# Kernel optimization log

Hardware: AMD Instinct MI355X
Metric: run time of the kernel (lower is better)

## Reference

```python
import jax, jax.numpy as jnp
import numpy as np
from jax import lax

B, G, P = 16, 128, 8000   # batch, MAX_GT_BOXES, num proposals
R = 200                   # train_rois_per_image
POS_CAP = int(R * 0.33)   # max positive rois per image = 66
BOX_STD = np.array([0.1, 0.1, 0.2, 0.2], np.float32)


def _make_boxes(k, shape):
    k1, k2, k3, k4 = jax.random.split(k, 4)
    y1 = jax.random.uniform(k1, shape) * 0.6
    x1 = jax.random.uniform(k2, shape) * 0.6
    h = jax.random.uniform(k3, shape) * 0.35 + 0.02
    w = jax.random.uniform(k4, shape) * 0.35 + 0.02
    return jnp.stack([y1, x1, y1 + h, x1 + w], axis=-1)


def setup_inputs() -> dict:
    key = jax.random.key(0)
    kg, kp, kc, kn, km = jax.random.split(key, 5)
    gt4 = _make_boxes(kg, (B, G))
    gt_cnt = jax.random.randint(kc, (B,), 5, G + 1)
    gt_tag = jnp.arange(G)[None, :] < gt_cnt[:, None]
    gt_boxes = jnp.concatenate([gt4, gt_tag[..., None].astype(jnp.float32)], axis=-1)
    cls = jax.random.randint(kn, (B, G), 1, 81)
    gt_class_ids = jnp.stack([cls * gt_tag, gt_tag.astype(jnp.int32)], axis=-1).astype(jnp.int32)
    pr4 = _make_boxes(kp, (B, P))
    pr_cnt = jax.random.randint(km, (B,), P // 2, P + 1)
    pr_tag = jnp.arange(P)[None, :] < pr_cnt[:, None]
    proposals = jnp.concatenate([pr4, pr_tag[..., None].astype(jnp.float32)], axis=-1)
    return {"gt_boxes": gt_boxes, "gt_class_ids": gt_class_ids, "proposals": proposals}


def _iou(gtb, prb):
    # gtb [G,4], prb [P,4] -> [G,P]
    iw = jnp.maximum(0.0, jnp.minimum(gtb[:, None, 3], prb[None, :, 3]) - jnp.maximum(gtb[:, None, 1], prb[None, :, 1]))
    ih = jnp.maximum(0.0, jnp.minimum(gtb[:, None, 2], prb[None, :, 2]) - jnp.maximum(gtb[:, None, 0], prb[None, :, 0]))
    inter = iw * ih
    ag = (gtb[:, 3] - gtb[:, 1]) * (gtb[:, 2] - gtb[:, 0])
    ap = (prb[:, 3] - prb[:, 1]) * (prb[:, 2] - prb[:, 0])
    return inter / (ag[:, None] + ap[None, :] - inter)


def _regress_target(anchors, gt):
    h = anchors[:, 2] - anchors[:, 0]
    w = anchors[:, 3] - anchors[:, 1]
    gh = gt[:, 2] - gt[:, 0]
    gw = gt[:, 3] - gt[:, 1]
    cy = (anchors[:, 2] + anchors[:, 0]) * 0.5
    cx = (anchors[:, 3] + anchors[:, 1]) * 0.5
    gcy = (gt[:, 2] + gt[:, 0]) * 0.5
    gcx = (gt[:, 3] + gt[:, 1]) * 0.5
    dy = (gcy - cy) / h
    dx = (gcx - cx) / w
    dh = jnp.log(jnp.maximum(gh / h, 1e-8))
    dw = jnp.log(jnp.maximum(gw / w, 1e-8))
    return jnp.stack([dy, dx, dh, dw], axis=1) / jnp.asarray(BOX_STD)


def _detect_targets_one(key, gt_boxes, gt_cls, proposals):
    valid_gt = gt_boxes[:, 4] != 0
    valid_pr = proposals[:, 4] != 0
    gtb = gt_boxes[:, :4]
    prb = proposals[:, :4]
    iou = jnp.where(valid_gt[:, None] & valid_pr[None, :], _iou(gtb, prb), -1.0)
    # remove each GT's best proposal from the candidate set (setdiff1d in original)
    gt_argmax = jnp.argmax(iou, axis=1)
    removed = jnp.zeros(P, jnp.int32).at[gt_argmax].max(valid_gt.astype(jnp.int32)) > 0
    iou2 = jnp.where(removed[None, :], -1.0, iou)
    p_max = iou2.max(axis=0)
    p_arg = jnp.argmax(iou2, axis=0)
    keep = (~removed) & valid_pr
    pos_m = keep & (p_max >= 0.5)
    neg_m = keep & (p_max < 0.5)
    # random subsampling (tf.random_shuffle) via uniform scores + top_k
    k1, k2 = jax.random.split(key)
    pos_idx = lax.top_k(jnp.where(pos_m, jax.random.uniform(k1, (P,)), -1.0), POS_CAP)[1]
    neg_idx = lax.top_k(jnp.where(neg_m, jax.random.uniform(k2, (P,)), -1.0), R)[1]
    n_pos = jnp.minimum(pos_m.sum(), POS_CAP)
    n_neg = jnp.minimum(R - n_pos, neg_m.sum())
    slot = jnp.arange(R)
    is_pos = slot < n_pos
    is_real = slot < n_pos + n_neg
    idx = jnp.where(is_pos, pos_idx[jnp.minimum(slot, POS_CAP - 1)], neg_idx[jnp.clip(slot - n_pos, 0, R - 1)])
    rois4 = jnp.where(is_real[:, None], prb[idx], 0.0)
    gsel = p_arg[idx]
    deltas4 = jnp.where(is_pos[:, None], _regress_target(prb[idx], gtb[gsel]), 0.0)
    cls = jnp.where(is_pos, gt_cls[gsel, 0].astype(jnp.float32), 0.0)
    delta_tag = jnp.where(is_pos, 1.0, jnp.where(is_real, -1.0, 0.0))
    deltas = jnp.concatenate([deltas4, delta_tag[:, None]], axis=1)      # [R,5]
    class_ids = jnp.stack([cls, is_real.astype(jnp.float32)], axis=1)    # [R,2]
    rois = jnp.concatenate([rois4, is_real[:, None].astype(jnp.float32)], axis=1)  # [R,5]
    matched = jnp.zeros(G, jnp.int32).at[p_arg].max(pos_m.astype(jnp.int32))
    miss = (valid_gt.sum() - (matched * valid_gt.astype(jnp.int32)).sum()).astype(jnp.float32)
    return deltas, class_ids, rois, miss


def reference(gt_boxes, gt_class_ids, proposals):
    keys = jax.random.split(jax.random.key(42), gt_boxes.shape[0])
    return jax.vmap(_detect_targets_one)(keys, gt_boxes, gt_class_ids, proposals)
```

## Files before the change

### kernel.cpp

```cpp
#include <hip/hip_runtime.h>
#include <stdint.h>

#define Bn 16
#define Gn 128
#define Pn 8000
#define Rn 200
#define POSCAP 66
#define CANDN 1024

typedef unsigned long long u64;

__device__ __forceinline__ void tf2x32(uint32_t k0, uint32_t k1,
                                       uint32_t x0, uint32_t x1,
                                       uint32_t& y0, uint32_t& y1) {
  uint32_t ks0 = k0, ks1 = k1, ks2 = k0 ^ k1 ^ 0x1BD11BDAu;
  x0 += ks0; x1 += ks1;
#define TF_ROUND(r) { x0 += x1; x1 = (x1 << (r)) | (x1 >> (32 - (r))); x1 ^= x0; }
  TF_ROUND(13) TF_ROUND(15) TF_ROUND(26) TF_ROUND(6)
  x0 += ks1; x1 += ks2 + 1u;
  TF_ROUND(17) TF_ROUND(29) TF_ROUND(16) TF_ROUND(24)
  x0 += ks2; x1 += ks0 + 2u;
  TF_ROUND(13) TF_ROUND(15) TF_ROUND(26) TF_ROUND(6)
  x0 += ks0; x1 += ks1 + 3u;
  TF_ROUND(17) TF_ROUND(29) TF_ROUND(16) TF_ROUND(24)
  x0 += ks1; x1 += ks2 + 4u;
  TF_ROUND(13) TF_ROUND(15) TF_ROUND(26) TF_ROUND(6)
  x0 += ks2; x1 += ks0 + 5u;
#undef TF_ROUND
  y0 = x0; y1 = x1;
}

__device__ __forceinline__ float iou_f(float g0, float g1, float g2, float g3, float ag,
                                       float p0, float p1, float p2, float p3) {
  float iw = fmaxf(0.0f, __fsub_rn(fminf(g3, p3), fmaxf(g1, p1)));
  float ih = fmaxf(0.0f, __fsub_rn(fminf(g2, p2), fmaxf(g0, p0)));
  float inter = __fmul_rn(iw, ih);
  float ap = __fmul_rn(__fsub_rn(p3, p1), __fsub_rn(p2, p0));
  return __fdiv_rn(inter, __fsub_rn(__fadd_rn(ag, ap), inter));
}

__global__ __launch_bounds__(256) void k_iou(const float* __restrict__ gt,
                                             const float* __restrict__ pr,
                                             float* __restrict__ pmax,
                                             int* __restrict__ parg,
                                             u64* __restrict__ rowpk) {
  __shared__ float sg[Gn * 5];
  __shared__ u64 srow[Gn];
  int b = blockIdx.y, tid = threadIdx.x;
  for (int i = tid; i < Gn * 5; i += 256) sg[i] = gt[(size_t)b * Gn * 5 + i];
  for (int i = tid; i < Gn; i += 256) srow[i] = 0ull;
  __syncthreads();
  int p = blockIdx.x * 256 + tid;
  float p0 = 0, p1 = 0, p2 = 0, p3 = 0, pv = 0;
  if (p < Pn) {
    const float* pb = pr + ((size_t)b * Pn + p) * 5;
    p0 = pb[0]; p1 = pb[1]; p2 = pb[2]; p3 = pb[3]; pv = pb[4];
  }
  bool valid = (p < Pn) && (pv != 0.0f);
  float best = -2.0f; int bidx = 0;
  int g0 = tid & (Gn - 1);
  for (int it = 0; it < Gn; it++) {
    int g = (g0 + it) & (Gn - 1);
    const float* gb = sg + g * 5;
    if (valid && gb[4] != 0.0f) {
      float ag = __fmul_rn(__fsub_rn(gb[3], gb[1]), __fsub_rn(gb[2], gb[0]));
      float v = iou_f(gb[0], gb[1], gb[2], gb[3], ag, p0, p1, p2, p3);
      if (v > best || (v == best && g < bidx)) { best = v; bidx = g; }
      u64 key = ((u64)__float_as_uint(v) << 32) | (unsigned)(~p);
      atomicMax(&srow[g], key);
    }
  }
  __syncthreads();
  for (int i = tid; i < Gn; i += 256) {
    u64 v = srow[i];
    if (v) atomicMax(&rowpk[(size_t)b * Gn + i], v);
  }
  if (p < Pn) {
    pmax[(size_t)b * Pn + p] = best;
    parg[(size_t)b * Pn + p] = bidx;
  }
}

__global__ __launch_bounds__(1024) void k_select(
    const float* __restrict__ gt, const int* __restrict__ gtc,
    const float* __restrict__ pr, const float* __restrict__ pmax,
    const int* __restrict__ parg, const u64* __restrict__ rowpk,
    float* __restrict__ out) {
  __shared__ uint32_t skey[Pn];
  __shared__ uint32_t hist2[1024];
  __shared__ uint32_t hist1[1024];
  __shared__ u64 cand[CANDN];
  __shared__ uint32_t rembm[Pn / 32 + 1];
  __shared__ int matched[Gn];
  __shared__ int s_npos, s_nneg, s_miss, s_call, s_cpos, s_T2, s_T1;
  __shared__ uint32_t s_keys[4];
  int b = blockIdx.x, tid = threadIdx.x;

  hist2[tid] = 0; hist1[tid] = 0; cand[tid] = 0ull;
  if (tid < Pn / 32 + 1) rembm[tid] = 0;
  if (tid < Gn) matched[tid] = 0;
  if (tid == 0) {
    s_npos = 0; s_nneg = 0; s_miss = 0; s_call = 0; s_cpos = 0;
    s_T2 = 1025; s_T1 = 1025;
    uint32_t kb0, kb1, a0, a1, c0, c1;
    tf2x32(0u, 42u, 0u, (uint32_t)b, kb0, kb1);
    tf2x32(kb0, kb1, 0u, 0u, a0, a1);
    tf2x32(kb0, kb1, 0u, 1u, c0, c1);
    s_keys[0] = a0; s_keys[1] = a1; s_keys[2] = c0; s_keys[3] = c1;
  }
  __syncthreads();

  if (tid < Gn) {
    float gv = gt[((size_t)b * Gn + tid) * 5 + 4];
    u64 pk = rowpk[(size_t)b * Gn + tid];
    if (gv != 0.0f && pk != 0ull) {
      unsigned p = ~(unsigned)(pk & 0xFFFFFFFFull);
      atomicOr(&rembm[p >> 5], 1u << (p & 31));
    }
  }
  __syncthreads();

  uint32_t k10 = s_keys[0], k11 = s_keys[1], k20 = s_keys[2], k21 = s_keys[3];
  const size_t bp = (size_t)b * Pn;
  int lpos = 0, lneg = 0;
  for (int p = tid; p < Pn; p += 1024) {
    float pv = pr[(bp + p) * 5 + 4];
    int rem = (rembm[p >> 5] >> (p & 31)) & 1;
    float pm = pmax[bp + p];
    int cls = 0;
    if (pv != 0.0f && !rem) cls = (pm >= 0.5f) ? 2 : 1;
    uint32_t key = 0;
    if (cls) {
      uint32_t kk0 = (cls == 2) ? k10 : k20, kk1 = (cls == 2) ? k11 : k21;
      uint32_t y0, y1;
      tf2x32(kk0, kk1, 0u, (uint32_t)p, y0, y1);
      uint32_t val = (y0 ^ y1) >> 9;
      key = ((uint32_t)cls << 23) | val;
      if (cls == 2) { lpos++; matched[parg[bp + p]] = 1; atomicAdd(&hist2[val >> 13], 1u); }
      else { lneg++; atomicAdd(&hist1[val >> 13], 1u); }
    }
    skey[p] = key;
  }
  if (lpos) atomicAdd(&s_npos, lpos);
  if (lneg) atomicAdd(&s_nneg, lneg);
  __syncthreads();

  if (tid < 128) {
    bool isP = tid < 64;
    int lane = tid & 63;
    uint32_t* hist = isP ? hist2 : hist1;
    int cnt = isP ? s_npos : s_nneg;
    int cap = isP ? POSCAP : Rn;
    int need = cnt < cap ? cnt : cap;
    int base = 1024 - 16 * (lane + 1);
    int local = 0;
#pragma unroll
    for (int j = 0; j < 16; j++) local += (int)hist[base + j];
    int incl = local;
    for (int d = 1; d < 64; d <<= 1) {
      int o = __shfl_up(incl, d);
      if (lane >= d) incl += o;
    }
    int above = incl - local;
    if (need > 0 && above < need && above + local >= need) {
      int cum = above, T = base;
      for (int j = 15; j >= 0; j--) {
        cum += (int)hist[base + j];
        if (cum >= need) { T = base + j; break; }
      }
      if (isP) s_T2 = T; else s_T1 = T;
    }
  }
  __syncthreads();
  int T2 = s_T2, T1 = s_T1;

  for (int p = tid; p < Pn; p += 1024) {
    uint32_t key = skey[p];
    int cls = (int)(key >> 23);
    if (cls) {
      int bucket = (int)((key & 0x7FFFFFu) >> 13);
      int T = (cls == 2) ? T2 : T1;
      if (bucket >= T) {
        int slot = atomicAdd(&s_call, 1);
        if (slot < CANDN) {
          cand[slot] = ((u64)key << 16) | (uint32_t)((uint16_t)(~p));
          if (cls == 2) atomicAdd(&s_cpos, 1);
        }
      }
    }
  }
  __syncthreads();

  for (unsigned k = 2; k <= CANDN; k <<= 1) {
    for (unsigned j = k >> 1; j > 0; j >>= 1) {
      unsigned i = tid, l = i ^ j;
      if (l > i) {
        u64 av = cand[i], cv = cand[l];
        bool a_first = av > cv;
        bool desc = ((i & k) == 0u);
        if (desc != a_first) { cand[i] = cv; cand[l] = av; }
      }
      __syncthreads();
    }
  }

  int npos = s_npos, nneg = s_nneg, cpos = s_cpos;
  int n_pos = npos < POSCAP ? npos : POSCAP;
  int rems = Rn - n_pos;
  int n_neg = nneg < rems ? nneg : rems;

  float* o_del = out;
  float* o_cls = out + (size_t)Bn * Rn * 5;
  float* o_roi = out + (size_t)Bn * Rn * 7;
  float* o_mis = out + (size_t)Bn * Rn * 12;

  if (tid < Rn) {
    int s = tid;
    bool is_pos = s < n_pos;
    bool is_real = s < n_pos + n_neg;
    float d0 = 0, d1 = 0, d2 = 0, d3 = 0, d4 = 0, c0 = 0, c1 = 0;
    float r0 = 0, r1 = 0, r2 = 0, r3 = 0, r4 = 0;
    if (is_real) {
      int ci = is_pos ? s : (cpos + (s - n_pos));
      u64 ck = cand[ci];
      int p = (int)((~(unsigned)ck) & 0xFFFFu);
      const float* pb = pr + (bp + p) * 5;
      float q0 = pb[0], q1 = pb[1], q2 = pb[2], q3 = pb[3];
      r0 = q0; r1 = q1; r2 = q2; r3 = q3; r4 = 1.0f; c1 = 1.0f;
      if (is_pos) {
        int g = parg[bp + p];
        const float* gb = gt + ((size_t)b * Gn + g) * 5;
        float g0 = gb[0], g1 = gb[1], g2 = gb[2], g3 = gb[3];
        float h = __fsub_rn(q2, q0), w = __fsub_rn(q3, q1);
        float gh = __fsub_rn(g2, g0), gw = __fsub_rn(g3, g1);
        float cy = __fmul_rn(__fadd_rn(q2, q0), 0.5f);
        float cx = __fmul_rn(__fadd_rn(q3, q1), 0.5f);
        float gcy = __fmul_rn(__fadd_rn(g2, g0), 0.5f);
        float gcx = __fmul_rn(__fadd_rn(g3, g1), 0.5f);
        float dy = __fdiv_rn(__fsub_rn(gcy, cy), h);
        float dx = __fdiv_rn(__fsub_rn(gcx, cx), w);
        float dh = logf(fmaxf(__fdiv_rn(gh, h), 1e-8f));
        float dw = logf(fmaxf(__fdiv_rn(gw, w), 1e-8f));
        d0 = __fdiv_rn(dy, 0.1f); d1 = __fdiv_rn(dx, 0.1f);
        d2 = __fdiv_rn(dh, 0.2f); d3 = __fdiv_rn(dw, 0.2f);
        d4 = 1.0f;
        c0 = (float)gtc[((size_t)b * Gn + g) * 2];
      } else {
        d4 = -1.0f;
      }
    }
    size_t ob = (size_t)b * Rn + s;
    o_del[ob * 5 + 0] = d0; o_del[ob * 5 + 1] = d1; o_del[ob * 5 + 2] = d2;
    o_del[ob * 5 + 3] = d3; o_del[ob * 5 + 4] = d4;
    o_cls[ob * 2 + 0] = c0; o_cls[ob * 2 + 1] = c1;
    o_roi[ob * 5 + 0] = r0; o_roi[ob * 5 + 1] = r1; o_roi[ob * 5 + 2] = r2;
    o_roi[ob * 5 + 3] = r3; o_roi[ob * 5 + 4] = r4;
  }

  if (tid < Gn) {
    float gv = gt[((size_t)b * Gn + tid) * 5 + 4];
    if (gv != 0.0f && matched[tid] == 0) atomicAdd(&s_miss, 1);
  }
  __syncthreads();
  if (tid == 0) o_mis[b] = (float)s_miss;
}

extern "C" void kernel_launch(void* const* d_in, const int* in_sizes, int n_in,
                              void* d_out, int out_size, void* d_ws, size_t ws_size,
                              hipStream_t stream) {
  const float* gt = (const float*)d_in[0];
  const int* gtc = (const int*)d_in[1];
  const float* pr = (const float*)d_in[2];
  float* out = (float*)d_out;

  u64* rowpk = (u64*)d_ws;
  float* pmax = (float*)(rowpk + Bn * Gn);
  int* parg = (int*)(pmax + (size_t)Bn * Pn);

  hipMemsetAsync(rowpk, 0, (size_t)Bn * Gn * sizeof(u64), stream);
  k_iou<<<dim3((Pn + 255) / 256, Bn), 256, 0, stream>>>(gt, pr, pmax, parg, rowpk);
  k_select<<<Bn, 1024, 0, stream>>>(gt, gtc, pr, pmax, parg, rowpk, out);
}
```

Baseline: 121.3 us.

## Split IoU into independent column-max and row-max block sets, drop shared atomics

The fused IoU kernel, which did per-element shared-memory 64-bit atomicMax for every GT row, is replaced by one launch with two kinds of blocks. Column blocks compute each proposal's best GT and pack the pos/neg label and argmax into a 16-bit word. Row blocks compute each GT's best proposal with a wavefront shuffle reduction. This removes the per-pair atomics, the memset and the float/int pmax/parg buffers, at the cost of computing every IoU twice and row blocks striding through global proposal data. Row blocks also now write a zero key for invalid GT rows, so the select kernel no longer checks the GT valid flag.

```diff
diff --git a/kernel.cpp b/kernel.cpp
--- a/kernel.cpp
+++ b/kernel.cpp
@@ -7,6 +7,8 @@
 #define Rn 200
 #define POSCAP 66
 #define CANDN 1024
+#define COLBLKS 512
+#define ROWBLKS 512
 
 typedef unsigned long long u64;
 
@@ -39,53 +41,69 @@
   return __fdiv_rn(inter, __fsub_rn(__fadd_rn(ag, ap), inter));
 }
 
-__global__ __launch_bounds__(256) void k_iou(const float* __restrict__ gt,
-                                             const float* __restrict__ pr,
-                                             float* __restrict__ pmax,
-                                             int* __restrict__ parg,
-                                             u64* __restrict__ rowpk) {
-  __shared__ float sg[Gn * 5];
-  __shared__ u64 srow[Gn];
-  int b = blockIdx.y, tid = threadIdx.x;
-  for (int i = tid; i < Gn * 5; i += 256) sg[i] = gt[(size_t)b * Gn * 5 + i];
-  for (int i = tid; i < Gn; i += 256) srow[i] = 0ull;
-  __syncthreads();
-  int p = blockIdx.x * 256 + tid;
-  float p0 = 0, p1 = 0, p2 = 0, p3 = 0, pv = 0;
-  if (p < Pn) {
+__global__ __launch_bounds__(256) void k_phase1(const float* __restrict__ gt,
+                                                const float* __restrict__ pr,
+                                                uint16_t* __restrict__ combo,
+                                                u64* __restrict__ rowpk) {
+  int bt = blockIdx.x, tid = threadIdx.x;
+  if (bt < COLBLKS) {
+    int b = bt >> 5;
+    int p = ((bt & 31) << 8) + tid;
+    if (p >= Pn) return;
     const float* pb = pr + ((size_t)b * Pn + p) * 5;
-    p0 = pb[0]; p1 = pb[1]; p2 = pb[2]; p3 = pb[3]; pv = pb[4];
-  }
-  bool valid = (p < Pn) && (pv != 0.0f);
-  float best = -2.0f; int bidx = 0;
-  int g0 = tid & (Gn - 1);
-  for (int it = 0; it < Gn; it++) {
-    int g = (g0 + it) & (Gn - 1);
-    const float* gb = sg + g * 5;
-    if (valid && gb[4] != 0.0f) {
-      float ag = __fmul_rn(__fsub_rn(gb[3], gb[1]), __fsub_rn(gb[2], gb[0]));
-      float v = iou_f(gb[0], gb[1], gb[2], gb[3], ag, p0, p1, p2, p3);
-      if (v > best || (v == best && g < bidx)) { best = v; bidx = g; }
-      u64 key = ((u64)__float_as_uint(v) << 32) | (unsigned)(~p);
-      atomicMax(&srow[g], key);
-    }
-  }
-  __syncthreads();
-  for (int i = tid; i < Gn; i += 256) {
-    u64 v = srow[i];
-    if (v) atomicMax(&rowpk[(size_t)b * Gn + i], v);
-  }
-  if (p < Pn) {
-    pmax[(size_t)b * Pn + p] = best;
-    parg[(size_t)b * Pn + p] = bidx;
+    float p0 = pb[0], p1 = pb[1], p2 = pb[2], p3 = pb[3], pv = pb[4];
+    int prelim = 0, bidx = 0;
+    if (pv != 0.0f) {
+      const float* gbase = gt + (size_t)b * Gn * 5;
+      float best = -2.0f;
+      for (int g = 0; g < Gn; g++) {
+        float gv = gbase[g * 5 + 4];
+        if (gv != 0.0f) {
+          float g0 = gbase[g * 5 + 0], g1 = gbase[g * 5 + 1];
+          float g2 = gbase[g * 5 + 2], g3 = gbase[g * 5 + 3];
+          float ag = __fmul_rn(__fsub_rn(g3, g1), __fsub_rn(g2, g0));
+          float v = iou_f(g0, g1, g2, g3, ag, p0, p1, p2, p3);
+          if (v > best) { best = v; bidx = g; }
+        }
+      }
+      prelim = (best >= 0.5f) ? 2 : 1;
+    }
+    combo[(size_t)b * Pn + p] = (uint16_t)((prelim << 8) | bidx);
+  } else {
+    int row = (bt - COLBLKS) * 4 + (tid >> 6);
+    int lane = tid & 63;
+    int b = row >> 7;
+    const float* gb = gt + (size_t)row * 5;
+    float gv = gb[4];
+    u64 key = 0;
+    if (gv != 0.0f) {
+      float g0 = gb[0], g1 = gb[1], g2 = gb[2], g3 = gb[3];
+      float ag = __fmul_rn(__fsub_rn(g3, g1), __fsub_rn(g2, g0));
+      const float* prb = pr + (size_t)b * Pn * 5;
+      float best = -2.0f; int bidx = 0;
+      for (int p = lane; p < Pn; p += 64) {
+        const float* pb = prb + (size_t)p * 5;
+        float pv = pb[4];
+        if (pv != 0.0f) {
+          float v = iou_f(g0, g1, g2, g3, ag, pb[0], pb[1], pb[2], pb[3]);
+          if (v > best) { best = v; bidx = p; }
+        }
+      }
+      for (int off = 32; off > 0; off >>= 1) {
+        float ov = __shfl_down(best, off);
+        int oi = __shfl_down(bidx, off);
+        if (ov > best || (ov == best && oi < bidx)) { best = ov; bidx = oi; }
+      }
+      key = ((u64)__float_as_uint(best) << 32) | (unsigned)(~bidx);
+    }
+    if (lane == 0) rowpk[row] = key;
   }
 }
 
 __global__ __launch_bounds__(1024) void k_select(
     const float* __restrict__ gt, const int* __restrict__ gtc,
-    const float* __restrict__ pr, const float* __restrict__ pmax,
-    const int* __restrict__ parg, const u64* __restrict__ rowpk,
-    float* __restrict__ out) {
+    const float* __restrict__ pr, const uint16_t* __restrict__ combo,
+    const u64* __restrict__ rowpk, float* __restrict__ out) {
   __shared__ uint32_t skey[Pn];
   __shared__ uint32_t hist2[1024];
   __shared__ uint32_t hist1[1024];
@@ -111,9 +129,8 @@
   __syncthreads();
 
   if (tid < Gn) {
-    float gv = gt[((size_t)b * Gn + tid) * 5 + 4];
     u64 pk = rowpk[(size_t)b * Gn + tid];
-    if (gv != 0.0f && pk != 0ull) {
+    if (pk != 0ull) {
       unsigned p = ~(unsigned)(pk & 0xFFFFFFFFull);
       atomicOr(&rembm[p >> 5], 1u << (p & 31));
     }
@@ -124,11 +141,9 @@
   const size_t bp = (size_t)b * Pn;
   int lpos = 0, lneg = 0;
   for (int p = tid; p < Pn; p += 1024) {
-    float pv = pr[(bp + p) * 5 + 4];
+    uint32_t cb = combo[bp + p];
     int rem = (rembm[p >> 5] >> (p & 31)) & 1;
-    float pm = pmax[bp + p];
-    int cls = 0;
-    if (pv != 0.0f && !rem) cls = (pm >= 0.5f) ? 2 : 1;
+    int cls = rem ? 0 : (int)(cb >> 8);
     uint32_t key = 0;
     if (cls) {
       uint32_t kk0 = (cls == 2) ? k10 : k20, kk1 = (cls == 2) ? k11 : k21;
@@ -136,7 +151,7 @@
       tf2x32(kk0, kk1, 0u, (uint32_t)p, y0, y1);
       uint32_t val = (y0 ^ y1) >> 9;
       key = ((uint32_t)cls << 23) | val;
-      if (cls == 2) { lpos++; matched[parg[bp + p]] = 1; atomicAdd(&hist2[val >> 13], 1u); }
+      if (cls == 2) { lpos++; matched[cb & 127] = 1; atomicAdd(&hist2[val >> 13], 1u); }
       else { lneg++; atomicAdd(&hist1[val >> 13], 1u); }
     }
     skey[p] = key;
@@ -228,7 +243,7 @@
       float q0 = pb[0], q1 = pb[1], q2 = pb[2], q3 = pb[3];
       r0 = q0; r1 = q1; r2 = q2; r3 = q3; r4 = 1.0f; c1 = 1.0f;
       if (is_pos) {
-        int g = parg[bp + p];
+        int g = (int)(combo[bp + p] & 127);
         const float* gb = gt + ((size_t)b * Gn + g) * 5;
         float g0 = gb[0], g1 = gb[1], g2 = gb[2], g3 = gb[3];
         float h = __fsub_rn(q2, q0), w = __fsub_rn(q3, q1);
@@ -274,10 +289,8 @@
   float* out = (float*)d_out;
 
   u64* rowpk = (u64*)d_ws;
-  float* pmax = (float*)(rowpk + Bn * Gn);
-  int* parg = (int*)(pmax + (size_t)Bn * Pn);
-
-  hipMemsetAsync(rowpk, 0, (size_t)Bn * Gn * sizeof(u64), stream);
-  k_iou<<<dim3((Pn + 255) / 256, Bn), 256, 0, stream>>>(gt, pr, pmax, parg, rowpk);
-  k_select<<<Bn, 1024, 0, stream>>>(gt, gtc, pr, pmax, parg, rowpk, out);
-}
+  uint16_t* combo = (uint16_t*)(rowpk + Bn * Gn);
+
+  k_phase1<<<COLBLKS + ROWBLKS, 256, 0, stream>>>(gt, pr, combo, rowpk);
+  k_select<<<Bn, 1024, 0, stream>>>(gt, gtc, pr, combo, rowpk, out);
+}
```

After: 144.5 us. 19.1% more time.
